# Kernel optimization log

Hardware: AMD Instinct MI355X
Metric: run time of the kernel (lower is better)

The kernel has to match this reference:

```python
import jax, jax.numpy as jnp
import numpy as np
import math

NUM_MODES = 7
NUM_KEYS = 12
DECAY = math.exp(-0.0005)
MAX_HEAT = 5.0
SEQ_LEN = 524288


def _build_weights():
    """Replicates HandcraftedKeyModel.__init__ weight construction -> [12, 84]."""
    base = np.array([1.5, 0.1, 0.6, 0.3, 0.8, 0.1, 0.2], dtype=np.float64)
    major_intervals = [2, 2, 1, 2, 2, 2, 1]
    W3 = np.empty((NUM_MODES, NUM_KEYS, NUM_KEYS), dtype=np.float32)
    for mode in range(NUM_MODES):
        ret = np.full(NUM_KEYS, 0.05, dtype=np.float64)
        offset = 0
        for i in range(NUM_MODES):
            ret[offset] = 1.0 / base[i]
            offset += major_intervals[(mode + i) % NUM_MODES]
        for scale in range(NUM_KEYS):
            # mode_w[scale:] ++ mode_w[:scale]  == left-rotation by `scale`
            W3[mode, scale] = np.roll(ret, -scale)
    # view(-1, 12).transpose(1, 0) -> [12, 84]
    return jnp.asarray(W3.reshape(-1, NUM_KEYS).T)


def setup_inputs() -> dict:
    key = jax.random.key(0)
    x = jax.random.randint(key, (1, SEQ_LEN), 0, 128, dtype=jnp.int32)
    W = _build_weights()  # [12, 84] fixed handcrafted weights
    return {"x": x, "W": W}


def reference(x, W):
    seq = x[0]  # [T] int notes
    T = seq.shape[0]
    valid = (seq > -10000).astype(W.dtype)  # sentinel test
    # one-hot increment per step: +1 at (note % 12) when valid  -> [T, 12]
    inc = jax.nn.one_hot(jnp.mod(seq, NUM_KEYS), NUM_KEYS, dtype=W.dtype) * valid[:, None]

    def step(h, inc_t):
        # decay, conditional scatter-add, clamp at max_heat (elementwise)
        h = jnp.minimum(h * jnp.asarray(DECAY, W.dtype) + inc_t, jnp.asarray(MAX_HEAT, W.dtype))
        return h, h

    _, heats = jax.lax.scan(step, jnp.zeros(NUM_KEYS, W.dtype), inc)  # [T, 12]
    # per-step tiny matmul [12] @ [12, 84] batched over the whole sequence
    out = (heats @ W).reshape(1, T, NUM_MODES, NUM_KEYS)
    return out
```

## Files before the change

kernel.cpp:

```cpp
#include <hip/hip_runtime.h>
#include <stdint.h>


#define NKEY 12
#define NOUT 84
#define LC   64
#define GROUPS 64

constexpr float DECAYF = 0.99950012497916927f;
constexpr float BIGC   = 1e30f;

constexpr float cpowf(float a, int n) {
    float r = 1.0f;
    for (int i = 0; i < n; ++i) r *= a;
    return r;
}
constexpr float A64F   = cpowf(DECAYF, LC);
constexpr float AG128F = cpowf(A64F, 128);

__global__ __launch_bounds__(128) void k_compose(const int* __restrict__ seq,
                                                 float* __restrict__ Bc,
                                                 float* __restrict__ Cc,
                                                 int nc) {
    int c = blockIdx.x * blockDim.x + threadIdx.x;
    if (c >= nc) return;
    const float D = DECAYF;
    float B[NKEY], C[NKEY];
#pragma unroll
    for (int k = 0; k < NKEY; ++k) { B[k] = 0.0f; C[k] = BIGC; }

    const int4* s4 = reinterpret_cast<const int4*>(seq) + c * (LC / 4);
    for (int q = 0; q < LC / 4; ++q) {
        int4 v4 = s4[q];
        int vv[4] = {v4.x, v4.y, v4.z, v4.w};
#pragma unroll
        for (int u = 0; u < 4; ++u) {
            int note = vv[u];
            bool valid = note > -10000;
            int m = note % NKEY; if (m < 0) m += NKEY;
#pragma unroll
            for (int k = 0; k < NKEY; ++k) {
                float b = (valid && (m == k)) ? 1.0f : 0.0f;
                B[k] = fmaf(B[k], D, b);
                C[k] = fminf(fmaf(C[k], D, b), 5.0f);
            }
        }
    }
#pragma unroll
    for (int k = 0; k < NKEY; ++k) {
        Bc[c * NKEY + k] = B[k];
        Cc[c * NKEY + k] = C[k];
    }
}

__global__ __launch_bounds__(GROUPS * NKEY) void k_scan(const float* __restrict__ Bc,
                                                        const float* __restrict__ Cc,
                                                        float* __restrict__ hstart,
                                                        int nc) {
    __shared__ float BG[GROUPS][NKEY], CG[GROUPS][NKEY];
    __shared__ float BP[GROUPS][NKEY], CP[GROUPS][NKEY];
    const int tid = threadIdx.x;
    const int g = tid / NKEY, k = tid % NKEY;
    const float A = A64F;
    const int per = nc / GROUPS;
    const float Ag = (per == 128) ? AG128F : __powf(A64F, (float)per);

    {
        float B = 0.0f, C = BIGC;
        int c0 = g * per;
        for (int i = 0; i < per; ++i) {
            float B1 = Bc[(c0 + i) * NKEY + k];
            float C1 = Cc[(c0 + i) * NKEY + k];
            B = fmaf(A, B, B1);
            C = fminf(fmaf(A, C, B1), C1);
        }
        BG[g][k] = B; CG[g][k] = C;
    }
    __syncthreads();

    if (tid < NKEY) {
        float B = 0.0f, C = BIGC;
        for (int g2 = 0; g2 < GROUPS; ++g2) {
            BP[g2][tid] = B; CP[g2][tid] = C;
            float B1 = BG[g2][tid], C1 = CG[g2][tid];
            B = fmaf(Ag, B, B1);
            C = fminf(fmaf(Ag, C, B1), C1);
        }
    }
    __syncthreads();

    {
        float B = BP[g][k], C = CP[g][k];
        int c0 = g * per;
        for (int i = 0; i < per; ++i) {
            hstart[(c0 + i) * NKEY + k] = fminf(B, C);
            float B1 = Bc[(c0 + i) * NKEY + k];
            float C1 = Cc[(c0 + i) * NKEY + k];
            B = fmaf(A, B, B1);
            C = fminf(fmaf(A, C, B1), C1);
        }
    }
}

__global__ __launch_bounds__(256) void k_out_fused(const int* __restrict__ seq,
                                                   const float* __restrict__ W,
                                                   const float* __restrict__ hstart,
                                                   float* __restrict__ out) {
    __shared__ float heats[LC][NKEY];
    __shared__ int   notes[LC];
    const int c   = blockIdx.x;
    const int tid = threadIdx.x;
    const int q = tid % 21;
    const int r = tid / 21;

    float4 w4[NKEY];
#pragma unroll
    for (int k = 0; k < NKEY; ++k)
        w4[k] = reinterpret_cast<const float4*>(W + k * NOUT)[q];

    if (tid < LC / 4) {
        int4 v = reinterpret_cast<const int4*>(seq + (size_t)c * LC)[tid];
        reinterpret_cast<int4*>(notes)[tid] = v;
    }
    if (tid < NKEY) {
        float h = hstart[c * NKEY + tid];
        const float D = DECAYF;
        for (int i = 0; i < LC; ++i) {
            int note = notes[i];
            bool valid = note > -10000;
            int m = note % NKEY; if (m < 0) m += NKEY;
            float b = (valid && (m == tid)) ? 1.0f : 0.0f;
            h = fminf(fmaf(h, D, b), 5.0f);
            heats[i][tid] = h;
        }
    }
    __syncthreads();
    if (tid >= 252) return;

    float* const op = out + (size_t)c * (LC * NOUT) + q * 4;

    auto emit_row = [&](int row) {
        const float4* hv = reinterpret_cast<const float4*>(&heats[row][0]);
        float4 h0 = hv[0], h1 = hv[1], h2 = hv[2];
        const float hk[NKEY] = {h0.x, h0.y, h0.z, h0.w,
                                h1.x, h1.y, h1.z, h1.w,
                                h2.x, h2.y, h2.z, h2.w};
        float4 o; o.x = o.y = o.z = o.w = 0.0f;
#pragma unroll
        for (int k = 0; k < NKEY; ++k) {
            o.x = fmaf(hk[k], w4[k].x, o.x);
            o.y = fmaf(hk[k], w4[k].y, o.y);
            o.z = fmaf(hk[k], w4[k].z, o.z);
            o.w = fmaf(hk[k], w4[k].w, o.w);
        }
        *reinterpret_cast<float4*>(op + row * NOUT) = o;
    };

#pragma unroll
    for (int s = 0; s < 5; ++s) emit_row(r + 12 * s);
    if (r < 4) emit_row(60 + r);
}

extern "C" void kernel_launch(void* const* d_in, const int* in_sizes, int n_in,
                              void* d_out, int out_size, void* d_ws, size_t ws_size,
                              hipStream_t stream) {
    const int*   seq = (const int*)d_in[0];
    const float* W   = (const float*)d_in[1];
    float*       out = (float*)d_out;

    const int T  = in_sizes[0];
    const int nc = T / LC;

    float* Bc = (float*)d_ws;
    float* Cc = Bc + (size_t)nc * NKEY;
    float* hs = Cc + (size_t)nc * NKEY;

    hipLaunchKernelGGL(k_compose, dim3((nc + 127) / 128), dim3(128), 0, stream,
                       seq, Bc, Cc, nc);
    hipLaunchKernelGGL(k_scan, dim3(1), dim3(GROUPS * NKEY), 0, stream,
                       Bc, Cc, hs, nc);
    hipLaunchKernelGGL(k_out_fused, dim3(nc), dim3(256), 0, stream,
                       seq, W, hs, out);
}
```

Measured before the change: 248.6 us.

## Restructure chunk-state scan into hierarchical group and super-group levels

The single-block scan over 8192 chunk summaries is replaced by three levels. Group summaries of 32 chunks are now built inside the compose kernel through shared memory. A second kernel then runs one block per key, scanning 256 groups in 16 super-groups and expanding per-chunk starting heats with 256 threads per key. Chunk summaries move to a key-major layout for coalesced per-key reads. The aim is to shorten the serial critical path of the single-block scan, at the cost of an extra shared-memory reduction in the compose kernel. The kernel now assumes nc is divisible by 128 and equals NGRP*GSZ.

Result: faster. 207.0 us (-16.8%).

```diff
diff --git a/kernel.cpp b/kernel.cpp
--- a/kernel.cpp
+++ b/kernel.cpp
@@ -5,25 +5,31 @@
 #define NKEY 12
 #define NOUT 84
 #define LC   64
-#define GROUPS 64
-
-constexpr float DECAYF = 0.99950012497916927f;
-constexpr float BIGC   = 1e30f;
-
-constexpr float cpowf(float a, int n) {
-    float r = 1.0f;
-    for (int i = 0; i < n; ++i) r *= a;
-    return r;
-}
-constexpr float A64F   = cpowf(DECAYF, LC);
-constexpr float AG128F = cpowf(A64F, 128);
-
-__global__ __launch_bounds__(128) void k_compose(const int* __restrict__ seq,
-                                                 float* __restrict__ Bc,
-                                                 float* __restrict__ Cc,
-                                                 int nc) {
-    int c = blockIdx.x * blockDim.x + threadIdx.x;
-    if (c >= nc) return;
+#define GSZ  32
+#define NGRP 256
+#define NSUP 16
+
+constexpr double DECAYD = 0.9995001249791693;
+constexpr float  DECAYF = (float)DECAYD;
+constexpr float  BIGC   = 1e30f;
+
+constexpr float cpowf(int n) {
+    double r = 1.0;
+    for (int i = 0; i < n; ++i) r *= DECAYD;
+    return (float)r;
+}
+constexpr float A64 = cpowf(LC);
+constexpr float AG  = cpowf(LC * GSZ);
+constexpr float AS  = cpowf(LC * GSZ * NSUP);
+
+__global__ __launch_bounds__(128) void kA(const int* __restrict__ seq,
+                                          float* __restrict__ Bc,
+                                          float* __restrict__ Cc,
+                                          float* __restrict__ BG,
+                                          float* __restrict__ CG,
+                                          int nc) {
+    const int tid = threadIdx.x;
+    const int c   = blockIdx.x * 128 + tid;
     const float D = DECAYF;
     float B[NKEY], C[NKEY];
 #pragma unroll
@@ -48,64 +54,87 @@
     }
 #pragma unroll
     for (int k = 0; k < NKEY; ++k) {
-        Bc[c * NKEY + k] = B[k];
-        Cc[c * NKEY + k] = C[k];
-    }
-}
-
-__global__ __launch_bounds__(GROUPS * NKEY) void k_scan(const float* __restrict__ Bc,
-                                                        const float* __restrict__ Cc,
-                                                        float* __restrict__ hstart,
-                                                        int nc) {
-    __shared__ float BG[GROUPS][NKEY], CG[GROUPS][NKEY];
-    __shared__ float BP[GROUPS][NKEY], CP[GROUPS][NKEY];
+        Bc[k * nc + c] = B[k];
+        Cc[k * nc + c] = C[k];
+    }
+
+    __shared__ float LB[128][NKEY], LX[128][NKEY];
+#pragma unroll
+    for (int k = 0; k < NKEY; ++k) { LB[tid][k] = B[k]; LX[tid][k] = C[k]; }
+    __syncthreads();
+    if (tid < 4 * NKEY) {
+        const int Gl = tid / NKEY, k = tid % NKEY;
+        float b = 0.0f, cc = BIGC;
+        const int base = Gl * GSZ;
+        for (int i = 0; i < GSZ; ++i) {
+            float b1 = LB[base + i][k], c1 = LX[base + i][k];
+            b  = fmaf(A64, b, b1);
+            cc = fminf(fmaf(A64, cc, b1), c1);
+        }
+        const int G = blockIdx.x * 4 + Gl;
+        BG[k * NGRP + G] = b;
+        CG[k * NGRP + G] = cc;
+    }
+}
+
+__global__ __launch_bounds__(256) void kB(const float* __restrict__ Bc,
+                                          const float* __restrict__ Cc,
+                                          const float* __restrict__ BG,
+                                          const float* __restrict__ CG,
+                                          float* __restrict__ hs,
+                                          int nc) {
+    const int k   = blockIdx.x;
     const int tid = threadIdx.x;
-    const int g = tid / NKEY, k = tid % NKEY;
-    const float A = A64F;
-    const int per = nc / GROUPS;
-    const float Ag = (per == 128) ? AG128F : __powf(A64F, (float)per);
-
+    __shared__ float SB[NSUP], SC[NSUP], PB[NSUP], PC[NSUP], VST[NGRP];
+
+    if (tid < NSUP) {
+        float b = 0.0f, c = BIGC;
+        for (int i = 0; i < NGRP / NSUP; ++i) {
+            const int G = tid * (NGRP / NSUP) + i;
+            float b1 = BG[k * NGRP + G], c1 = CG[k * NGRP + G];
+            b = fmaf(AG, b, b1);
+            c = fminf(fmaf(AG, c, b1), c1);
+        }
+        SB[tid] = b; SC[tid] = c;
+    }
+    __syncthreads();
+    if (tid == 0) {
+        float b = 0.0f, c = BIGC;
+        for (int s = 0; s < NSUP; ++s) {
+            PB[s] = b; PC[s] = c;
+            float b1 = SB[s], c1 = SC[s];
+            b = fmaf(AS, b, b1);
+            c = fminf(fmaf(AS, c, b1), c1);
+        }
+    }
+    __syncthreads();
+    if (tid < NSUP) {
+        float b = PB[tid], c = PC[tid];
+        for (int i = 0; i < NGRP / NSUP; ++i) {
+            const int G = tid * (NGRP / NSUP) + i;
+            VST[G] = fminf(b, c);
+            float b1 = BG[k * NGRP + G], c1 = CG[k * NGRP + G];
+            b = fmaf(AG, b, b1);
+            c = fminf(fmaf(AG, c, b1), c1);
+        }
+    }
+    __syncthreads();
     {
-        float B = 0.0f, C = BIGC;
-        int c0 = g * per;
-        for (int i = 0; i < per; ++i) {
-            float B1 = Bc[(c0 + i) * NKEY + k];
-            float C1 = Cc[(c0 + i) * NKEY + k];
-            B = fmaf(A, B, B1);
-            C = fminf(fmaf(A, C, B1), C1);
-        }
-        BG[g][k] = B; CG[g][k] = C;
-    }
-    __syncthreads();
-
-    if (tid < NKEY) {
-        float B = 0.0f, C = BIGC;
-        for (int g2 = 0; g2 < GROUPS; ++g2) {
-            BP[g2][tid] = B; CP[g2][tid] = C;
-            float B1 = BG[g2][tid], C1 = CG[g2][tid];
-            B = fmaf(Ag, B, B1);
-            C = fminf(fmaf(Ag, C, B1), C1);
-        }
-    }
-    __syncthreads();
-
-    {
-        float B = BP[g][k], C = CP[g][k];
-        int c0 = g * per;
-        for (int i = 0; i < per; ++i) {
-            hstart[(c0 + i) * NKEY + k] = fminf(B, C);
-            float B1 = Bc[(c0 + i) * NKEY + k];
-            float C1 = Cc[(c0 + i) * NKEY + k];
-            B = fmaf(A, B, B1);
-            C = fminf(fmaf(A, C, B1), C1);
-        }
-    }
-}
-
-__global__ __launch_bounds__(256) void k_out_fused(const int* __restrict__ seq,
-                                                   const float* __restrict__ W,
-                                                   const float* __restrict__ hstart,
-                                                   float* __restrict__ out) {
+        const int g = tid;
+        float v = VST[g];
+        const int c0 = g * GSZ;
+        for (int i = 0; i < GSZ; ++i) {
+            hs[(size_t)(c0 + i) * NKEY + k] = v;
+            float b1 = Bc[k * nc + c0 + i], c1 = Cc[k * nc + c0 + i];
+            v = fminf(fmaf(A64, v, b1), c1);
+        }
+    }
+}
+
+__global__ __launch_bounds__(256) void kC(const int* __restrict__ seq,
+                                          const float* __restrict__ W,
+                                          const float* __restrict__ hs,
+                                          float* __restrict__ out) {
     __shared__ float heats[LC][NKEY];
     __shared__ int   notes[LC];
     const int c   = blockIdx.x;
@@ -123,7 +152,7 @@
         reinterpret_cast<int4*>(notes)[tid] = v;
     }
     if (tid < NKEY) {
-        float h = hstart[c * NKEY + tid];
+        float h = hs[(size_t)c * NKEY + tid];
         const float D = DECAYF;
         for (int i = 0; i < LC; ++i) {
             int note = notes[i];
@@ -172,13 +201,15 @@
     const int nc = T / LC;
 
     float* Bc = (float*)d_ws;
-    float* Cc = Bc + (size_t)nc * NKEY;
-    float* hs = Cc + (size_t)nc * NKEY;
-
-    hipLaunchKernelGGL(k_compose, dim3((nc + 127) / 128), dim3(128), 0, stream,
-                       seq, Bc, Cc, nc);
-    hipLaunchKernelGGL(k_scan, dim3(1), dim3(GROUPS * NKEY), 0, stream,
-                       Bc, Cc, hs, nc);
-    hipLaunchKernelGGL(k_out_fused, dim3(nc), dim3(256), 0, stream,
+    float* Cc = Bc + (size_t)NKEY * nc;
+    float* BG = Cc + (size_t)NKEY * nc;
+    float* CG = BG + (size_t)NKEY * NGRP;
+    float* hs = CG + (size_t)NKEY * NGRP;
+
+    hipLaunchKernelGGL(kA, dim3(nc / 128), dim3(128), 0, stream,
+                       seq, Bc, Cc, BG, CG, nc);
+    hipLaunchKernelGGL(kB, dim3(NKEY), dim3(NGRP), 0, stream,
+                       Bc, Cc, BG, CG, hs, nc);
+    hipLaunchKernelGGL(kC, dim3(nc), dim3(256), 0, stream,
                        seq, W, hs, out);
 }
```

## Fold chunk-group scan into compose kernel and drop single-block scan launch

Applied to the files above, without the earlier changes.

Removes the single-block scan kernel. The compose kernel now performs an intra-block scan over its 128 chunks and writes per-chunk local prefixes plus a per-group aggregate. The output kernel recomputes the cross-group prefix itself by folding up to 63 group aggregates before seeding its heat recurrence. This trades a serialized one-block launch for redundant prefix work in every output block. It also hardcodes 64 groups of 128 chunks, so it assumes the sequence length and computes the decay powers in double precision.

Measured after the change: 224.3 us. 1.11x faster.

```diff
diff --git a/kernel.cpp b/kernel.cpp
--- a/kernel.cpp
+++ b/kernel.cpp
@@ -5,25 +5,28 @@
 #define NKEY 12
 #define NOUT 84
 #define LC   64
-#define GROUPS 64
+#define CPG  128
+#define NGRP 64
 
-constexpr float DECAYF = 0.99950012497916927f;
-constexpr float BIGC   = 1e30f;
+constexpr double DECAYD = 0.9995001249791693;
+constexpr float  DECAYF = (float)DECAYD;
+constexpr float  BIGC   = 1e30f;
 
-constexpr float cpowf(float a, int n) {
-    float r = 1.0f;
-    for (int i = 0; i < n; ++i) r *= a;
-    return r;
+constexpr float cpowf(int n) {
+    double r = 1.0;
+    for (int i = 0; i < n; ++i) r *= DECAYD;
+    return (float)r;
 }
-constexpr float A64F   = cpowf(DECAYF, LC);
-constexpr float AG128F = cpowf(A64F, 128);
+constexpr float A64 = cpowf(LC);
+constexpr float AG  = cpowf(LC * CPG);
 
-__global__ __launch_bounds__(128) void k_compose(const int* __restrict__ seq,
-                                                 float* __restrict__ Bc,
-                                                 float* __restrict__ Cc,
-                                                 int nc) {
-    int c = blockIdx.x * blockDim.x + threadIdx.x;
-    if (c >= nc) return;
+__global__ __launch_bounds__(CPG) void k1(const int* __restrict__ seq,
+                                          float* __restrict__ loc,
+                                          float* __restrict__ agg,
+                                          float* __restrict__ Atab) {
+    __shared__ float LB[CPG][13], LX[CPG][13];
+    const int t = threadIdx.x;
+    const int c = blockIdx.x * CPG + t;
     const float D = DECAYF;
     float B[NKEY], C[NKEY];
 #pragma unroll
@@ -47,65 +50,33 @@
         }
     }
 #pragma unroll
-    for (int k = 0; k < NKEY; ++k) {
-        Bc[c * NKEY + k] = B[k];
-        Cc[c * NKEY + k] = C[k];
+    for (int k = 0; k < NKEY; ++k) { LB[t][k] = B[k]; LX[t][k] = C[k]; }
+    __syncthreads();
+
+    if (t < NKEY) {
+        float b = 0.0f, cc = BIGC, a = 1.0f;
+        const int base = blockIdx.x * CPG;
+        const bool w0 = (blockIdx.x == 0) && (t == 0);
+        for (int j = 0; j < CPG; ++j) {
+            loc[(size_t)(base + j) * 24 + t]      = b;
+            loc[(size_t)(base + j) * 24 + 12 + t] = cc;
+            if (w0) Atab[j] = a;
+            a *= A64;
+            float b1 = LB[j][t], c1 = LX[j][t];
+            b  = fmaf(A64, b, b1);
+            cc = fminf(fmaf(A64, cc, b1), c1);
+        }
+        agg[blockIdx.x * 24 + t]      = b;
+        agg[blockIdx.x * 24 + 12 + t] = cc;
     }
 }
 
-__global__ __launch_bounds__(GROUPS * NKEY) void k_scan(const float* __restrict__ Bc,
-                                                        const float* __restrict__ Cc,
-                                                        float* __restrict__ hstart,
-                                                        int nc) {
-    __shared__ float BG[GROUPS][NKEY], CG[GROUPS][NKEY];
-    __shared__ float BP[GROUPS][NKEY], CP[GROUPS][NKEY];
-    const int tid = threadIdx.x;
-    const int g = tid / NKEY, k = tid % NKEY;
-    const float A = A64F;
-    const int per = nc / GROUPS;
-    const float Ag = (per == 128) ? AG128F : __powf(A64F, (float)per);
-
-    {
-        float B = 0.0f, C = BIGC;
-        int c0 = g * per;
-        for (int i = 0; i < per; ++i) {
-            float B1 = Bc[(c0 + i) * NKEY + k];
-            float C1 = Cc[(c0 + i) * NKEY + k];
-            B = fmaf(A, B, B1);
-            C = fminf(fmaf(A, C, B1), C1);
-        }
-        BG[g][k] = B; CG[g][k] = C;
-    }
-    __syncthreads();
-
-    if (tid < NKEY) {
-        float B = 0.0f, C = BIGC;
-        for (int g2 = 0; g2 < GROUPS; ++g2) {
-            BP[g2][tid] = B; CP[g2][tid] = C;
-            float B1 = BG[g2][tid], C1 = CG[g2][tid];
-            B = fmaf(Ag, B, B1);
-            C = fminf(fmaf(Ag, C, B1), C1);
-        }
-    }
-    __syncthreads();
-
-    {
-        float B = BP[g][k], C = CP[g][k];
-        int c0 = g * per;
-        for (int i = 0; i < per; ++i) {
-            hstart[(c0 + i) * NKEY + k] = fminf(B, C);
-            float B1 = Bc[(c0 + i) * NKEY + k];
-            float C1 = Cc[(c0 + i) * NKEY + k];
-            B = fmaf(A, B, B1);
-            C = fminf(fmaf(A, C, B1), C1);
-        }
-    }
-}
-
-__global__ __launch_bounds__(256) void k_out_fused(const int* __restrict__ seq,
-                                                   const float* __restrict__ W,
-                                                   const float* __restrict__ hstart,
-                                                   float* __restrict__ out) {
+__global__ __launch_bounds__(256) void kC(const int* __restrict__ seq,
+                                          const float* __restrict__ W,
+                                          const float* __restrict__ loc,
+                                          const float* __restrict__ agg,
+                                          const float* __restrict__ Atab,
+                                          float* __restrict__ out) {
     __shared__ float heats[LC][NKEY];
     __shared__ int   notes[LC];
     const int c   = blockIdx.x;
@@ -123,7 +94,12 @@
         reinterpret_cast<int4*>(notes)[tid] = v;
     }
     if (tid < NKEY) {
-        float h = hstart[c * NKEY + tid];
+        const int g = c >> 7, j = c & (CPG - 1);
+        float v = 0.0f;
+        for (int gp = 0; gp < g; ++gp)
+            v = fminf(fmaf(AG, v, agg[gp * 24 + tid]), agg[gp * 24 + 12 + tid]);
+        float h = fminf(fmaf(Atab[j], v, loc[(size_t)c * 24 + tid]),
+                        loc[(size_t)c * 24 + 12 + tid]);
         const float D = DECAYF;
         for (int i = 0; i < LC; ++i) {
             int note = notes[i];
@@ -171,14 +147,12 @@
     const int T  = in_sizes[0];
     const int nc = T / LC;
 
-    float* Bc = (float*)d_ws;
-    float* Cc = Bc + (size_t)nc * NKEY;
-    float* hs = Cc + (size_t)nc * NKEY;
+    float* loc  = (float*)d_ws;
+    float* agg  = loc + (size_t)nc * 24;
+    float* Atab = agg + (size_t)NGRP * 24;
 
-    hipLaunchKernelGGL(k_compose, dim3((nc + 127) / 128), dim3(128), 0, stream,
-                       seq, Bc, Cc, nc);
-    hipLaunchKernelGGL(k_scan, dim3(1), dim3(GROUPS * NKEY), 0, stream,
-                       Bc, Cc, hs, nc);
-    hipLaunchKernelGGL(k_out_fused, dim3(nc), dim3(256), 0, stream,
-                       seq, W, hs, out);
+    hipLaunchKernelGGL(k1, dim3(NGRP), dim3(CPG), 0, stream,
+                       seq, loc, agg, Atab);
+    hipLaunchKernelGGL(kC, dim3(nc), dim3(256), 0, stream,
+                       seq, W, loc, agg, Atab, out);
 }
```
